# Optimization experiments

Measured on AMD Instinct MI355X. Metric: run time of the kernel, lower is better.

Reference implementation:

```python
import jax, jax.numpy as jnp
import numpy as np

B, L, D_IN = 4, 2048, 1024
D_KEY, D_VAL = 1024, 1024
N_SLOTS, TOPK = 32768, 16
TEMP = 0.1
EPS = 1e-5


def layer_norm(x, g, b):
    mu = jnp.mean(x, axis=-1, keepdims=True)
    var = jnp.var(x, axis=-1, keepdims=True)
    return (x - mu) * jax.lax.rsqrt(var + EPS) * g + b


def setup_inputs() -> dict:
    key = jax.random.key(0)
    ks = jax.random.split(key, 8)
    s_in = 1.0 / np.sqrt(D_IN)
    s_ft = 1.0 / np.sqrt(D_IN + D_VAL + 1)
    return {
        "h_in": jax.random.normal(ks[0], (B, L, D_IN), jnp.float32),
        "Wk": jax.random.normal(ks[1], (D_IN, D_KEY), jnp.float32) * s_in,
        "bk": jnp.zeros((D_KEY,), jnp.float32),
        "cube_keys": jax.random.normal(ks[2], (N_SLOTS, D_KEY), jnp.float32),
        "cube_vals": jax.random.normal(ks[3], (N_SLOTS, D_VAL), jnp.float32) * 0.1,
        "ln_in_g": jnp.ones((D_IN,), jnp.float32),
        "ln_in_b": jnp.zeros((D_IN,), jnp.float32),
        "ln_pred_g": jnp.ones((D_VAL,), jnp.float32),
        "ln_pred_b": jnp.zeros((D_VAL,), jnp.float32),
        "W1": jax.random.normal(ks[4], (D_IN + D_VAL + 1, D_IN), jnp.float32) * s_ft,
        "b1": jnp.zeros((D_IN,), jnp.float32),
        "W2": jax.random.normal(ks[5], (D_IN, 1), jnp.float32) * s_in,
        "b2": jnp.zeros((1,), jnp.float32),
    }


def reference(h_in, Wk, bk, cube_keys, cube_vals, ln_in_g, ln_in_b,
              ln_pred_g, ln_pred_b, W1, b1, W2, b2):
    Bv, Lv, Dv = h_in.shape
    # key projection -> [B*L, d_key]
    keys = (jnp.einsum('bld,dk->blk', h_in, Wk) + bk).reshape(Bv * Lv, -1)
    # cube kNN query: cosine similarity against slot keys
    kn = keys * jax.lax.rsqrt(jnp.sum(keys * keys, -1, keepdims=True) + 1e-8)
    mn = cube_keys * jax.lax.rsqrt(jnp.sum(cube_keys * cube_keys, -1, keepdims=True) + 1e-8)
    sims = kn @ mn.T                                   # [BL, N]
    top_sims, idx = jax.lax.top_k(sims, TOPK)          # [BL, K]
    w = jax.nn.softmax(top_sims / TEMP, axis=-1)       # retrieval weights
    vals = jnp.take(cube_vals, idx, axis=0)            # [BL, K, d_val] gather
    pred = jnp.einsum('nk,nkd->nd', w, vals).reshape(Bv, Lv, -1)
    conf = ((top_sims[:, 0] + 1.0) * 0.5).reshape(Bv, Lv, 1)
    # gate
    feats = jnp.concatenate([layer_norm(h_in, ln_in_g, ln_in_b),
                             layer_norm(pred, ln_pred_g, ln_pred_b),
                             conf], axis=-1)
    hmid = jax.nn.silu(jnp.einsum('blf,fd->bld', feats, W1) + b1)
    alpha = jnp.clip(jax.nn.sigmoid(jnp.einsum('bld,do->blo', hmid, W2) + b2), 0.0, 1.0)
    # blend (y_teacher is None): (1-a)*h + a*(h+pred)
    y_out = (1.0 - alpha) * h_in + alpha * (h_in + pred)
    return y_out, jnp.mean(alpha), jnp.mean(conf)
```

## Files before the change

### kernel.cpp

```cpp
#include <hip/hip_runtime.h>
#include <hip/hip_bf16.h>
#include <cstdint>
#include <cstddef>

typedef __bf16 bf16;
typedef __bf16 bf16x4 __attribute__((ext_vector_type(4)));
typedef __bf16 bf16x8 __attribute__((ext_vector_type(8)));
typedef float  f32x4  __attribute__((ext_vector_type(4)));

#define BL      8192
#define DDIM    1024
#define NSLOTS  32768
#define NSPLIT  8
#define SLOTS_PER (NSLOTS / NSPLIT)
#define CAP     49

#define WS_MN    ((size_t)0)
#define WS_PRED  ((size_t)0)
#define WS_HBF   ((size_t)67108864)
#define WS_HMID  WS_HBF
#define WS_WKT   ((size_t)83886080)
#define WS_W1T   ((size_t)85983232)
#define WS_KEYS  ((size_t)90177536)
#define WS_FEATS WS_KEYS
#define WS_KN    ((size_t)123731968)
#define WS_TPK   ((size_t)140509184)
#define WS_CONF  ((size_t)148897792)

__device__ __forceinline__ void async16(const void* g, void* l) {
  __builtin_amdgcn_global_load_lds(
      (const __attribute__((address_space(1))) void*)g,
      (__attribute__((address_space(3))) void*)(uintptr_t)(uint32_t)(uintptr_t)l,
      16, 0, 0);
}

__device__ __forceinline__ void stage_tile(const bf16* __restrict__ src, int ld,
                                           bf16* lds, int tid) {
  const int wave = tid >> 6;
#pragma unroll
  for (int issue = 0; issue < 2; ++issue) {
    const int gi  = issue * 256 + tid;
    const int row = gi >> 2;
    const int gc  = (gi & 3) ^ ((gi >> 3) & 3);
    const bf16* g = src + (size_t)row * ld + gc * 8;
    bf16* l = lds + (size_t)(issue * 256 + wave * 64) * 8;
    async16(g, l);
  }
}

__device__ __forceinline__ f32x4 mfma_bf16(bf16x8 a, bf16x8 b, f32x4 c) {
  return __builtin_amdgcn_mfma_f32_16x16x32_bf16(a, b, c, 0, 0, 0);
}

__device__ __forceinline__ float block_sum(float v, float* red) {
#pragma unroll
  for (int off = 32; off > 0; off >>= 1) v += __shfl_xor(v, off, 64);
  const int tid = threadIdx.x;
  if ((tid & 63) == 0) red[tid >> 6] = v;
  __syncthreads();
  v = red[0] + red[1] + red[2] + red[3];
  __syncthreads();
  return v;
}

__device__ __forceinline__ uint32_t pack_key(float v, int slot) {
  return ((__float_as_uint(v) ^ 0x80000000u) & 0xFFFF8000u) | (uint32_t)slot;
}

__device__ __forceinline__ void drain_merge(uint32_t* cand, int* cnt, int rb_own,
                                            uint32_t (&tk)[16], float& thrF) {
  int n = cnt[rb_own];
  n = n > CAP ? CAP : n;
  for (int t = 0;; ++t) {
    if (!__any(t < n)) break;
    uint32_t cur = 0u;
    if (t < n) cur = cand[rb_own * CAP + t];
#pragma unroll
    for (int p = 0; p < 16; ++p) {
      const uint32_t old = tk[p];
      const uint32_t mx = old > cur ? old : cur;
      tk[p] = mx;
      cur = old > cur ? cur : old;
    }
  }
  cnt[rb_own] = 0;
  thrF = __uint_as_float((tk[15] & 0xFFFF8000u) ^ 0x80000000u);
}

__global__ void cvt_bf16_kernel(const float* __restrict__ in, bf16* __restrict__ out, int n4) {
  int i = blockIdx.x * blockDim.x + threadIdx.x;
  if (i >= n4) return;
  f32x4 v = *(const f32x4*)(in + (size_t)i * 4);
  bf16x4 o = {(bf16)v.x, (bf16)v.y, (bf16)v.z, (bf16)v.w};
  *(bf16x4*)(out + (size_t)i * 4) = o;
}

__global__ void transpose_f32_bf16(const float* __restrict__ in, bf16* __restrict__ out,
                                   int R, int C) {
  __shared__ float tile[32][33];
  const int c0 = blockIdx.x * 32, r0 = blockIdx.y * 32;
  for (int i = threadIdx.y; i < 32; i += 8)
    tile[i][threadIdx.x] = in[(size_t)(r0 + i) * C + c0 + threadIdx.x];
  __syncthreads();
  for (int i = threadIdx.y; i < 32; i += 8)
    out[(size_t)(c0 + i) * R + r0 + threadIdx.x] = (bf16)tile[threadIdx.x][i];
}

__global__ __launch_bounds__(256) void rownorm_kernel(const float* __restrict__ in,
                                                      bf16* __restrict__ out) {
  __shared__ float red[4];
  const int row = blockIdx.x, t = threadIdx.x;
  f32x4 v = *(const f32x4*)(in + (size_t)row * 1024 + t * 4);
  float sq = v.x * v.x + v.y * v.y + v.z * v.z + v.w * v.w;
  sq = block_sum(sq, red);
  float sc = rsqrtf(sq + 1e-8f);
  bf16x4 o = {(bf16)(v.x * sc), (bf16)(v.y * sc), (bf16)(v.z * sc), (bf16)(v.w * sc)};
  *(bf16x4*)(out + (size_t)row * 1024 + t * 4) = o;
}

template <int EPI>
__global__ __launch_bounds__(256, 2) void gemm_bt_kernel(
    const bf16* __restrict__ A, const bf16* __restrict__ Bm, int Kd,
    float* __restrict__ Cf, bf16* __restrict__ Cb,
    const float* __restrict__ bias, const float* __restrict__ conf,
    const float* __restrict__ w1c) {
  __shared__ bf16 As0[128 * 32];
  __shared__ bf16 As1[128 * 32];
  __shared__ bf16 Bs0[128 * 32];
  __shared__ bf16 Bs1[128 * 32];
  const int tid = threadIdx.x;
  const int lane = tid & 63, wave = tid >> 6;
  const int wr = (wave >> 1) * 64, wc = (wave & 1) * 64;
  const int m0 = blockIdx.x * 128, n0 = blockIdx.y * 128;
  const int ar = lane & 15;
  const int sw8 = (((lane >> 4) ^ ((ar >> 1) & 3)) << 3);

  f32x4 acc[4][4];
#pragma unroll
  for (int i = 0; i < 4; ++i)
#pragma unroll
    for (int j = 0; j < 4; ++j) acc[i][j] = (f32x4){0.f, 0.f, 0.f, 0.f};

  const bf16 *Ac = As0, *An = As1, *Bc = Bs0, *Bn = Bs1;
  const int NT = Kd >> 5;
  stage_tile(A + (size_t)m0 * Kd, Kd, (bf16*)Ac, tid);
  stage_tile(Bm + (size_t)n0 * Kd, Kd, (bf16*)Bc, tid);

  for (int T = 0; T < NT; ++T) {
    if (T + 1 < NT) {
      stage_tile(A + (size_t)m0 * Kd + (T + 1) * 32, Kd, (bf16*)An, tid);
      stage_tile(Bm + (size_t)n0 * Kd + (T + 1) * 32, Kd, (bf16*)Bn, tid);
      asm volatile("s_waitcnt vmcnt(4)" ::: "memory");
    } else {
      asm volatile("s_waitcnt vmcnt(0)" ::: "memory");
    }
    __builtin_amdgcn_s_barrier();
    bf16x8 af[4], bfr[4];
#pragma unroll
    for (int i = 0; i < 4; ++i)
      af[i] = *(const bf16x8*)(Ac + (wr + i * 16 + ar) * 32 + sw8);
#pragma unroll
    for (int j = 0; j < 4; ++j)
      bfr[j] = *(const bf16x8*)(Bc + (wc + j * 16 + ar) * 32 + sw8);
#pragma unroll
    for (int i = 0; i < 4; ++i)
#pragma unroll
      for (int j = 0; j < 4; ++j)
        acc[i][j] = mfma_bf16(af[i], bfr[j], acc[i][j]);
    asm volatile("s_waitcnt lgkmcnt(0)" ::: "memory");
    __builtin_amdgcn_s_barrier();
    const bf16* t0 = Ac; Ac = An; An = t0;
    const bf16* t1 = Bc; Bc = Bn; Bn = t1;
  }

  const int mq = (lane >> 4) * 4, nq = lane & 15;
#pragma unroll
  for (int i = 0; i < 4; ++i)
#pragma unroll
    for (int j = 0; j < 4; ++j)
#pragma unroll
      for (int r = 0; r < 4; ++r) {
        const int m = m0 + wr + i * 16 + mq + r;
        const int n = n0 + wc + j * 16 + nq;
        float x = acc[i][j][r];
        if (EPI == 0) {
          Cf[(size_t)m * 1024 + n] = x + bias[n];
        } else {
          x += bias[n] + conf[m] * w1c[n];
          x = x / (1.f + expf(-x));
          Cb[(size_t)m * 1024 + n] = (bf16)x;
        }
      }
}

__global__ __launch_bounds__(256, 2) void sims_topk_kernel(
    const bf16* __restrict__ kn, const bf16* __restrict__ mn,
    uint32_t* __restrict__ tpk) {
  __shared__ bf16 As[128 * 32];
  __shared__ bf16 Bs0[128 * 32];
  __shared__ bf16 Bs1[128 * 32];
  __shared__ uint32_t cand[256 * CAP];
  __shared__ int cnt[256];

  const int tid = threadIdx.x;
  const int lane = tid & 63, wave = tid >> 6;
  const int wr = (wave >> 1) * 64;
  const int ch = wave & 1;
  const int split = blockIdx.x;
  const int m0 = blockIdx.y * 128;
  const int sbeg = split * SLOTS_PER;
  const int ar = lane & 15;
  const int sw8 = (((lane >> 4) ^ ((ar >> 1) & 3)) << 3);
  const int mq = (lane >> 4) * 4, nq = lane & 15;
  const int rb_own = (wr + lane) * 2 + ch;

  cnt[tid] = 0;

  uint32_t tk[16];
#pragma unroll
  for (int j = 0; j < 16; ++j) tk[j] = 0u;
  float thrF = __uint_as_float(0x80000000u);

  for (int it = 0; it < SLOTS_PER / 256; ++it) {
    f32x4 acc[2][4][4];
#pragma unroll
    for (int c = 0; c < 2; ++c)
#pragma unroll
      for (int i = 0; i < 4; ++i)
#pragma unroll
        for (int j = 0; j < 4; ++j) acc[c][i][j] = (f32x4){0.f, 0.f, 0.f, 0.f};

    const int n0 = sbeg + it * 256;
    for (int k0 = 0; k0 < 1024; k0 += 32) {
      __syncthreads();
      stage_tile(kn + (size_t)m0 * 1024 + k0, 1024, As, tid);
      stage_tile(mn + (size_t)n0 * 1024 + k0, 1024, Bs0, tid);
      stage_tile(mn + (size_t)(n0 + 128) * 1024 + k0, 1024, Bs1, tid);
      __syncthreads();
      bf16x8 af[4], b0[4], b1[4];
#pragma unroll
      for (int i = 0; i < 4; ++i)
        af[i] = *(const bf16x8*)(As + (wr + i * 16 + ar) * 32 + sw8);
#pragma unroll
      for (int j = 0; j < 4; ++j) {
        b0[j] = *(const bf16x8*)(Bs0 + (ch * 64 + j * 16 + ar) * 32 + sw8);
        b1[j] = *(const bf16x8*)(Bs1 + (ch * 64 + j * 16 + ar) * 32 + sw8);
      }
#pragma unroll
      for (int i = 0; i < 4; ++i)
#pragma unroll
        for (int j = 0; j < 4; ++j) {
          acc[0][i][j] = mfma_bf16(af[i], b0[j], acc[0][i][j]);
          acc[1][i][j] = mfma_bf16(af[i], b1[j], acc[1][i][j]);
        }
    }

#pragma unroll
    for (int cc = 0; cc < 2; ++cc) {
      const int colbase = sbeg + it * 256 + cc * 128 + ch * 64;
      uint64_t skip = 0ull;
#pragma unroll
      for (int i = 0; i < 4; ++i)
#pragma unroll
        for (int r = 0; r < 4; ++r) {
          const int owner = i * 16 + mq + r;
          const float thr = __shfl(thrF, owner, 64);
          const int rb = (wr + owner) * 2 + ch;
#pragma unroll
          for (int j = 0; j < 4; ++j) {
            const float v = acc[cc][i][j][r];
            if (v > thr) {
              const int old = atomicAdd(&cnt[rb], 1);
              if (old < CAP) cand[rb * CAP + old] = pack_key(v, colbase + j * 16 + nq);
              else skip |= (1ull << (i * 16 + r * 4 + j));
            }
          }
        }
      drain_merge(cand, cnt, rb_own, tk, thrF);
      if (__any(skip != 0ull)) {
#pragma unroll
        for (int i = 0; i < 4; ++i)
#pragma unroll
          for (int r = 0; r < 4; ++r) {
            const int owner = i * 16 + mq + r;
            const float thr = __shfl(thrF, owner, 64);
            const int rb = (wr + owner) * 2 + ch;
#pragma unroll
            for (int j = 0; j < 4; ++j) {
              if (skip & (1ull << (i * 16 + r * 4 + j))) {
                const float v = acc[cc][i][j][r];
                if (v > thr) {
                  const int old = atomicAdd(&cnt[rb], 1);
                  if (old < CAP) cand[rb * CAP + old] = pack_key(v, colbase + j * 16 + nq);
                }
              }
            }
          }
        drain_merge(cand, cnt, rb_own, tk, thrF);
      }
    }
  }

  const int row = m0 + wr + lane;
  uint32_t* dst = tpk + (((size_t)row * NSPLIT + split) * 2 + ch) * 16;
#pragma unroll
  for (int j = 0; j < 16; ++j) dst[j] = tk[j];
}

__global__ __launch_bounds__(256) void merge_pred_kernel(
    const uint32_t* __restrict__ tpk, const float* __restrict__ vals,
    float* __restrict__ pred, float* __restrict__ conf) {
  __shared__ uint32_t ks[256];
  __shared__ float sv[16];
  __shared__ int si[16];
  __shared__ float sw[16];
  const int row = blockIdx.x, t = threadIdx.x;
  const uint32_t k = tpk[(size_t)row * 256 + t];
  ks[t] = k;
  __syncthreads();
  int rank = 0;
  for (int j = 0; j < 256; ++j) rank += (ks[j] > k);
  if (rank < 16) {
    sv[rank] = __uint_as_float((k & 0xFFFF8000u) ^ 0x80000000u);
    si[rank] = (int)(k & 0x7FFFu);
  }
  __syncthreads();
  if (t == 0) {
    const float m = sv[0];
    float s = 0.f;
#pragma unroll
    for (int q = 0; q < 16; ++q) {
      float e = expf((sv[q] - m) * 10.f);
      sw[q] = e;
      s += e;
    }
    const float inv = 1.f / s;
#pragma unroll
    for (int q = 0; q < 16; ++q) sw[q] *= inv;
    conf[row] = (m + 1.f) * 0.5f;
  }
  __syncthreads();
  const int col = t * 4;
  f32x4 a = (f32x4){0.f, 0.f, 0.f, 0.f};
#pragma unroll
  for (int q = 0; q < 16; ++q) {
    f32x4 vv = *(const f32x4*)(vals + (size_t)si[q] * 1024 + col);
    a += vv * sw[q];
  }
  *(f32x4*)(pred + (size_t)row * 1024 + col) = a;
}

__global__ __launch_bounds__(256) void feats_kernel(
    const float* __restrict__ h, const float* __restrict__ pred,
    const float* __restrict__ gin, const float* __restrict__ bin,
    const float* __restrict__ gpr, const float* __restrict__ bpr,
    bf16* __restrict__ feats) {
  __shared__ float red[4];
  const int row = blockIdx.x, t = threadIdx.x;
  {
    f32x4 v = *(const f32x4*)(h + (size_t)row * 1024 + t * 4);
    float s = v.x + v.y + v.z + v.w;
    float sq = v.x * v.x + v.y * v.y + v.z * v.z + v.w * v.w;
    s = block_sum(s, red);
    sq = block_sum(sq, red);
    const float mean = s * (1.f / 1024.f);
    const float rstd = rsqrtf(sq * (1.f / 1024.f) - mean * mean + 1e-5f);
    f32x4 g = *(const f32x4*)(gin + t * 4);
    f32x4 b = *(const f32x4*)(bin + t * 4);
    bf16x4 o = {(bf16)((v.x - mean) * rstd * g.x + b.x),
                (bf16)((v.y - mean) * rstd * g.y + b.y),
                (bf16)((v.z - mean) * rstd * g.z + b.z),
                (bf16)((v.w - mean) * rstd * g.w + b.w)};
    *(bf16x4*)(feats + (size_t)row * 2048 + t * 4) = o;
  }
  {
    f32x4 v = *(const f32x4*)(pred + (size_t)row * 1024 + t * 4);
    float s = v.x + v.y + v.z + v.w;
    float sq = v.x * v.x + v.y * v.y + v.z * v.z + v.w * v.w;
    s = block_sum(s, red);
    sq = block_sum(sq, red);
    const float mean = s * (1.f / 1024.f);
    const float rstd = rsqrtf(sq * (1.f / 1024.f) - mean * mean + 1e-5f);
    f32x4 g = *(const f32x4*)(gpr + t * 4);
    f32x4 b = *(const f32x4*)(bpr + t * 4);
    bf16x4 o = {(bf16)((v.x - mean) * rstd * g.x + b.x),
                (bf16)((v.y - mean) * rstd * g.y + b.y),
                (bf16)((v.z - mean) * rstd * g.z + b.z),
                (bf16)((v.w - mean) * rstd * g.w + b.w)};
    *(bf16x4*)(feats + (size_t)row * 2048 + 1024 + t * 4) = o;
  }
}

__global__ __launch_bounds__(256) void final_kernel(
    const bf16* __restrict__ hmid, const float* __restrict__ W2,
    const float* __restrict__ b2, const float* __restrict__ h,
    const float* __restrict__ pred, const float* __restrict__ conf,
    float* __restrict__ out) {
  __shared__ float red[4];
  const int row = blockIdx.x, t = threadIdx.x;
  float s = 0.f;
#pragma unroll
  for (int j = 0; j < 4; ++j) {
    const int c = t + 256 * j;
    s += (float)hmid[(size_t)row * 1024 + c] * W2[c];
  }
  s = block_sum(s, red);
  float alpha = 1.f / (1.f + expf(-(s + b2[0])));
  alpha = fminf(fmaxf(alpha, 0.f), 1.f);
  f32x4 hv = *(const f32x4*)(h + (size_t)row * 1024 + t * 4);
  f32x4 pv = *(const f32x4*)(pred + (size_t)row * 1024 + t * 4);
  f32x4 y = hv + pv * alpha;
  *(f32x4*)(out + (size_t)row * 1024 + t * 4) = y;
  if (t == 0) {
    atomicAdd(out + 8388608, alpha * (1.f / 8192.f));
    atomicAdd(out + 8388609, conf[row] * (1.f / 8192.f));
  }
}

extern "C" void kernel_launch(void* const* d_in, const int* in_sizes, int n_in,
                              void* d_out, int out_size, void* d_ws, size_t ws_size,
                              hipStream_t stream) {
  const float* h_in      = (const float*)d_in[0];
  const float* Wk        = (const float*)d_in[1];
  const float* bk        = (const float*)d_in[2];
  const float* cube_keys = (const float*)d_in[3];
  const float* cube_vals = (const float*)d_in[4];
  const float* ln_in_g   = (const float*)d_in[5];
  const float* ln_in_b   = (const float*)d_in[6];
  const float* ln_pred_g = (const float*)d_in[7];
  const float* ln_pred_b = (const float*)d_in[8];
  const float* W1        = (const float*)d_in[9];
  const float* b1        = (const float*)d_in[10];
  const float* W2        = (const float*)d_in[11];
  const float* b2        = (const float*)d_in[12];

  char* ws = (char*)d_ws;
  bf16*     mn    = (bf16*)(ws + WS_MN);
  float*    pred  = (float*)(ws + WS_PRED);
  bf16*     h_bf  = (bf16*)(ws + WS_HBF);
  bf16*     hmid  = (bf16*)(ws + WS_HMID);
  bf16*     wkT   = (bf16*)(ws + WS_WKT);
  bf16*     w1T   = (bf16*)(ws + WS_W1T);
  float*    keys  = (float*)(ws + WS_KEYS);
  bf16*     feats = (bf16*)(ws + WS_FEATS);
  bf16*     kn    = (bf16*)(ws + WS_KN);
  uint32_t* tpk   = (uint32_t*)(ws + WS_TPK);
  float*    conf  = (float*)(ws + WS_CONF);
  float*    out   = (float*)d_out;
  const float* w1c = W1 + (size_t)2048 * 1024;

  cvt_bf16_kernel<<<(BL * DDIM / 4 + 255) / 256, 256, 0, stream>>>(h_in, h_bf, BL * DDIM / 4);
  transpose_f32_bf16<<<dim3(32, 32), dim3(32, 8), 0, stream>>>(Wk, wkT, 1024, 1024);
  transpose_f32_bf16<<<dim3(32, 64), dim3(32, 8), 0, stream>>>(W1, w1T, 2048, 1024);
  rownorm_kernel<<<NSLOTS, 256, 0, stream>>>(cube_keys, mn);

  gemm_bt_kernel<0><<<dim3(64, 8), 256, 0, stream>>>(h_bf, wkT, 1024, keys, nullptr,
                                                     bk, nullptr, nullptr);
  rownorm_kernel<<<BL, 256, 0, stream>>>(keys, kn);

  sims_topk_kernel<<<dim3(NSPLIT, 64), 256, 0, stream>>>(kn, mn, tpk);

  merge_pred_kernel<<<BL, 256, 0, stream>>>(tpk, cube_vals, pred, conf);

  feats_kernel<<<BL, 256, 0, stream>>>(h_in, pred, ln_in_g, ln_in_b,
                                       ln_pred_g, ln_pred_b, feats);
  gemm_bt_kernel<1><<<dim3(64, 8), 256, 0, stream>>>(feats, w1T, 2048, nullptr, hmid,
                                                     b1, conf, w1c);

  hipMemsetAsync(out + 8388608, 0, 8, stream);
  final_kernel<<<BL, 256, 0, stream>>>(hmid, W2, b2, h_in, pred, conf, out);
}
```

Baseline: 1.406 ms.

## Double K-tile depth in sims/top-k GEMM and shrink candidate buffer

The sims_topk kernel now stages 64-wide K tiles with an 8-way XOR swizzle, halving the number of barrier-synchronized staging rounds per output tile. To keep LDS usage fitting two blocks per CU, the per-row candidate capacity drops from 49 to 17. The overflow path becomes a loop so candidates that overflow the smaller buffer are retried until all are merged. The trade-off is more frequent drain/merge passes when many candidates pass the threshold, especially early in the scan.

```diff
diff --git a/kernel.cpp b/kernel.cpp
--- a/kernel.cpp
+++ b/kernel.cpp
@@ -13,7 +13,7 @@
 #define NSLOTS  32768
 #define NSPLIT  8
 #define SLOTS_PER (NSLOTS / NSPLIT)
-#define CAP     49
+#define CAP     17
 
 #define WS_MN    ((size_t)0)
 #define WS_PRED  ((size_t)0)
@@ -42,6 +42,20 @@
     const int gi  = issue * 256 + tid;
     const int row = gi >> 2;
     const int gc  = (gi & 3) ^ ((gi >> 3) & 3);
+    const bf16* g = src + (size_t)row * ld + gc * 8;
+    bf16* l = lds + (size_t)(issue * 256 + wave * 64) * 8;
+    async16(g, l);
+  }
+}
+
+__device__ __forceinline__ void stage_tile64(const bf16* __restrict__ src, int ld,
+                                             bf16* lds, int tid) {
+  const int wave = tid >> 6;
+#pragma unroll
+  for (int issue = 0; issue < 4; ++issue) {
+    const int gi  = issue * 256 + tid;
+    const int row = gi >> 3;
+    const int gc  = (gi & 7) ^ ((gi >> 3) & 7);
     const bf16* g = src + (size_t)row * ld + gc * 8;
     bf16* l = lds + (size_t)(issue * 256 + wave * 64) * 8;
     async16(g, l);
@@ -196,9 +210,9 @@
 __global__ __launch_bounds__(256, 2) void sims_topk_kernel(
     const bf16* __restrict__ kn, const bf16* __restrict__ mn,
     uint32_t* __restrict__ tpk) {
-  __shared__ bf16 As[128 * 32];
-  __shared__ bf16 Bs0[128 * 32];
-  __shared__ bf16 Bs1[128 * 32];
+  __shared__ bf16 As[128 * 64];
+  __shared__ bf16 Bs0[128 * 64];
+  __shared__ bf16 Bs1[128 * 64];
   __shared__ uint32_t cand[256 * CAP];
   __shared__ int cnt[256];
 
@@ -209,9 +223,9 @@
   const int split = blockIdx.x;
   const int m0 = blockIdx.y * 128;
   const int sbeg = split * SLOTS_PER;
-  const int ar = lane & 15;
-  const int sw8 = (((lane >> 4) ^ ((ar >> 1) & 3)) << 3);
-  const int mq = (lane >> 4) * 4, nq = lane & 15;
+  const int ar = lane & 15, g4 = lane >> 4;
+  const int a7 = ar & 7;
+  const int mq = g4 * 4, nq = lane & 15;
   const int rb_own = (wr + lane) * 2 + ch;
 
   cnt[tid] = 0;
@@ -231,28 +245,32 @@
         for (int j = 0; j < 4; ++j) acc[c][i][j] = (f32x4){0.f, 0.f, 0.f, 0.f};
 
     const int n0 = sbeg + it * 256;
-    for (int k0 = 0; k0 < 1024; k0 += 32) {
+    for (int k0 = 0; k0 < 1024; k0 += 64) {
       __syncthreads();
-      stage_tile(kn + (size_t)m0 * 1024 + k0, 1024, As, tid);
-      stage_tile(mn + (size_t)n0 * 1024 + k0, 1024, Bs0, tid);
-      stage_tile(mn + (size_t)(n0 + 128) * 1024 + k0, 1024, Bs1, tid);
+      stage_tile64(kn + (size_t)m0 * 1024 + k0, 1024, As, tid);
+      stage_tile64(mn + (size_t)n0 * 1024 + k0, 1024, Bs0, tid);
+      stage_tile64(mn + (size_t)(n0 + 128) * 1024 + k0, 1024, Bs1, tid);
       __syncthreads();
-      bf16x8 af[4], b0[4], b1[4];
-#pragma unroll
-      for (int i = 0; i < 4; ++i)
-        af[i] = *(const bf16x8*)(As + (wr + i * 16 + ar) * 32 + sw8);
-#pragma unroll
-      for (int j = 0; j < 4; ++j) {
-        b0[j] = *(const bf16x8*)(Bs0 + (ch * 64 + j * 16 + ar) * 32 + sw8);
-        b1[j] = *(const bf16x8*)(Bs1 + (ch * 64 + j * 16 + ar) * 32 + sw8);
+#pragma unroll
+      for (int ks = 0; ks < 2; ++ks) {
+        const int ca = (((ks << 2) | g4) ^ a7) << 3;
+        bf16x8 af[4], b0[4], b1[4];
+#pragma unroll
+        for (int i = 0; i < 4; ++i)
+          af[i] = *(const bf16x8*)(As + (wr + i * 16 + ar) * 64 + ca);
+#pragma unroll
+        for (int j = 0; j < 4; ++j) {
+          b0[j] = *(const bf16x8*)(Bs0 + (ch * 64 + j * 16 + ar) * 64 + ca);
+          b1[j] = *(const bf16x8*)(Bs1 + (ch * 64 + j * 16 + ar) * 64 + ca);
+        }
+#pragma unroll
+        for (int i = 0; i < 4; ++i)
+#pragma unroll
+          for (int j = 0; j < 4; ++j) {
+            acc[0][i][j] = mfma_bf16(af[i], b0[j], acc[0][i][j]);
+            acc[1][i][j] = mfma_bf16(af[i], b1[j], acc[1][i][j]);
+          }
       }
-#pragma unroll
-      for (int i = 0; i < 4; ++i)
-#pragma unroll
-        for (int j = 0; j < 4; ++j) {
-          acc[0][i][j] = mfma_bf16(af[i], b0[j], acc[0][i][j]);
-          acc[1][i][j] = mfma_bf16(af[i], b1[j], acc[1][i][j]);
-        }
     }
 
 #pragma unroll
@@ -277,7 +295,8 @@
           }
         }
       drain_merge(cand, cnt, rb_own, tk, thrF);
-      if (__any(skip != 0ull)) {
+      while (__any(skip != 0ull)) {
+        uint64_t ns = 0ull;
 #pragma unroll
         for (int i = 0; i < 4; ++i)
 #pragma unroll
@@ -292,11 +311,13 @@
                 if (v > thr) {
                   const int old = atomicAdd(&cnt[rb], 1);
                   if (old < CAP) cand[rb * CAP + old] = pack_key(v, colbase + j * 16 + nq);
+                  else ns |= (1ull << (i * 16 + r * 4 + j));
                 }
               }
             }
           }
         drain_merge(cand, cnt, rb_own, tk, thrF);
+        skip = ns;
       }
     }
   }
```

After: 1.946 ms. 1.38x slower.

## Double slot splits, shrink candidate buffer, merge half-wave top-k in LDS

Applied to the files above, without the earlier changes.

Doubles the number of slot splits so each block scans fewer slots. The candidate capacity drops to 17 and the buffer is drained after every 4x4 sub-tile, which removes the overflow/skip retry path. The two per-row top-16 lists held by the column halves are merged in LDS before writing, so each split writes one list instead of two. Draining more often adds synchronisation and merge work inside the inner loop, and the new column base (n0) depends on code outside the shown hunk.

```diff
diff --git a/kernel.cpp b/kernel.cpp
--- a/kernel.cpp
+++ b/kernel.cpp
@@ -11,9 +11,9 @@
 #define BL      8192
 #define DDIM    1024
 #define NSLOTS  32768
-#define NSPLIT  8
+#define NSPLIT  16
 #define SLOTS_PER (NSLOTS / NSPLIT)
-#define CAP     49
+#define CAP     17
 
 #define WS_MN    ((size_t)0)
 #define WS_PRED  ((size_t)0)
@@ -257,54 +257,52 @@
 
 #pragma unroll
     for (int cc = 0; cc < 2; ++cc) {
-      const int colbase = sbeg + it * 256 + cc * 128 + ch * 64;
-      uint64_t skip = 0ull;
-#pragma unroll
-      for (int i = 0; i < 4; ++i)
-#pragma unroll
-        for (int r = 0; r < 4; ++r) {
-          const int owner = i * 16 + mq + r;
-          const float thr = __shfl(thrF, owner, 64);
-          const int rb = (wr + owner) * 2 + ch;
-#pragma unroll
-          for (int j = 0; j < 4; ++j) {
+      const int colbase = n0 + cc * 128 + ch * 64;
+#pragma unroll
+      for (int i = 0; i < 4; ++i) {
+#pragma unroll
+        for (int j = 0; j < 4; ++j) {
+#pragma unroll
+          for (int r = 0; r < 4; ++r) {
+            const int owner = i * 16 + mq + r;
+            const float thr = __shfl(thrF, owner, 64);
+            const int rb = (wr + owner) * 2 + ch;
             const float v = acc[cc][i][j][r];
             if (v > thr) {
               const int old = atomicAdd(&cnt[rb], 1);
               if (old < CAP) cand[rb * CAP + old] = pack_key(v, colbase + j * 16 + nq);
-              else skip |= (1ull << (i * 16 + r * 4 + j));
             }
           }
+          drain_merge(cand, cnt, rb_own, tk, thrF);
         }
-      drain_merge(cand, cnt, rb_own, tk, thrF);
-      if (__any(skip != 0ull)) {
-#pragma unroll
-        for (int i = 0; i < 4; ++i)
-#pragma unroll
-          for (int r = 0; r < 4; ++r) {
-            const int owner = i * 16 + mq + r;
-            const float thr = __shfl(thrF, owner, 64);
-            const int rb = (wr + owner) * 2 + ch;
-#pragma unroll
-            for (int j = 0; j < 4; ++j) {
-              if (skip & (1ull << (i * 16 + r * 4 + j))) {
-                const float v = acc[cc][i][j][r];
-                if (v > thr) {
-                  const int old = atomicAdd(&cnt[rb], 1);
-                  if (old < CAP) cand[rb * CAP + old] = pack_key(v, colbase + j * 16 + nq);
-                }
-              }
-            }
-          }
-        drain_merge(cand, cnt, rb_own, tk, thrF);
       }
     }
   }
 
-  const int row = m0 + wr + lane;
-  uint32_t* dst = tpk + (((size_t)row * NSPLIT + split) * 2 + ch) * 16;
-#pragma unroll
-  for (int j = 0; j < 16; ++j) dst[j] = tk[j];
+  __syncthreads();
+  uint32_t* xbuf = cand;
+  if (ch == 1) {
+#pragma unroll
+    for (int j = 0; j < 16; ++j) xbuf[(wr + lane) * 17 + j] = tk[j];
+  }
+  __syncthreads();
+  if (ch == 0) {
+#pragma unroll
+    for (int j = 0; j < 16; ++j) {
+      uint32_t cur = xbuf[(wr + lane) * 17 + j];
+#pragma unroll
+      for (int p = 0; p < 16; ++p) {
+        const uint32_t old = tk[p];
+        const uint32_t mx = old > cur ? old : cur;
+        tk[p] = mx;
+        cur = old > cur ? cur : old;
+      }
+    }
+    const int row = m0 + wr + lane;
+    uint32_t* dst = tpk + ((size_t)row * NSPLIT + split) * 16;
+#pragma unroll
+    for (int j = 0; j < 16; ++j) dst[j] = tk[j];
+  }
 }
 
 __global__ __launch_bounds__(256) void merge_pred_kernel(
```

New measurement: 1.714 ms. +21.9%, slower.
